# Kernel optimization log

Measured on AMD Instinct MI355X. Metric: run time of the kernel, lower is better.

## Reference

```python
import jax, jax.numpy as jnp
import numpy as np

L, S, N, E, H = 2048, 2048, 4, 512, 8
D = E // H


def _rel_shift(x):
    # Faithful replication of the torch code's _rel_shift (which keeps [:1],
    # collapsing the S axis to size 1): x is (L, N, H, S) -> (L, N, H, 1).
    l, n, h, s = x.shape
    pad = jnp.concatenate([x, jnp.zeros((l, n, h, 1), x.dtype)], axis=-1)  # L,N,H,S+1
    p = jnp.transpose(pad, (0, 3, 1, 2))  # L,S+1,N,H  ('lnhs->lsnh')
    # view([S+1, L, N, H])[:1] == first L*N*H flat elements reshaped to (1,L,N,H)
    p = p.reshape(-1)[: l * n * h].reshape(1, l, n, h)
    return jnp.transpose(p, (1, 2, 3, 0))  # 'slnh->lnhs' -> (L,N,H,1)


def setup_inputs() -> dict:
    key = jax.random.key(0)
    ks = jax.random.split(key, 9)
    sc_in = (2.0 / (E + 3 * E)) ** 0.5  # xavier-ish scale
    sc_sq = (1.0 / E) ** 0.5
    return {
        "query": jax.random.normal(ks[0], (L, N, E), jnp.float32),
        "key": jax.random.normal(ks[1], (S, N, E), jnp.float32),
        "value": jax.random.normal(ks[2], (S, N, E), jnp.float32),
        "sin_pos_enc": jax.random.normal(ks[3], (S, E), jnp.float32),
        "in_proj_weight": jax.random.normal(ks[4], (3 * E, E), jnp.float32) * sc_in,
        "in_proj_bias": jnp.zeros((3 * E,), jnp.float32),
        "out_w": jax.random.normal(ks[5], (E, E), jnp.float32) * sc_sq,
        "out_b": jnp.zeros((E,), jnp.float32),
        "rel_proj_w": jax.random.normal(ks[6], (E, E), jnp.float32) * sc_sq,
        "rel_u": jax.random.normal(ks[7], (H, D), jnp.float32) * 0.1,
        "rel_v": jax.random.normal(ks[8], (H, D), jnp.float32) * 0.1,
    }


def reference(query, key, value, sin_pos_enc, in_proj_weight, in_proj_bias,
              out_w, out_b, rel_proj_w, rel_u, rel_v):
    def src_proj(x, base):
        w = in_proj_weight[base * E:(base + 1) * E]
        b = in_proj_bias[base * E:(base + 1) * E]
        y = x @ w.T + b  # T,N,E
        return y.reshape(y.shape[0], -1, H, D)  # T,N,H,D

    q = src_proj(query, 0)   # L,N,H,D
    k = src_proj(key, 1)     # S,N,H,D
    v = src_proj(value, 2)   # S,N,H,D
    rel_pos = (sin_pos_enc @ rel_proj_w.T).reshape(S, H, D)  # S,H,D

    term_ac = jnp.einsum('lnhd,snhd->lnhs', q + rel_u, k)      # L,N,H,S
    term_bd = jnp.einsum('lnhd,shd->lnhs', q + rel_v, rel_pos) # L,N,H,S
    term_bd = _rel_shift(term_bd)                              # L,N,H,1

    att = jax.nn.softmax((term_ac + term_bd) / (D ** 0.5), axis=-1)  # L,N,H,S
    out = jnp.einsum('lnhs,snhd->lnhd', att, v).reshape(L, -1, E)    # L,N,E
    out = out @ out_w.T + out_b
    att_weights = jnp.transpose(att.mean(axis=-2), (1, 0, 2))  # N,L,S
    return (out, att_weights)
```

## Files before the change

### kernel.cpp

```cpp
#include <hip/hip_runtime.h>
#include <hip/hip_bf16.h>
#include <stdint.h>


#define L_Q 2048
#define S_K 2048
#define N_B 4
#define E_D 512
#define H_N 8
#define D_H 64

typedef unsigned short u16;
typedef unsigned int u32;
typedef short v8s __attribute__((ext_vector_type(8)));
typedef float v4f __attribute__((ext_vector_type(4)));

#define MFMA16(a, b, c) __builtin_amdgcn_mfma_f32_16x16x32_bf16(a, b, c, 0, 0, 0)

__device__ __forceinline__ float bf2f(u16 u) {
  unsigned int x = ((unsigned int)u) << 16;
  return __builtin_bit_cast(float, x);
}
__device__ __forceinline__ u16 f2bf(float f) {
  unsigned int x = __builtin_bit_cast(unsigned int, f);
  x += 0x7FFFu + ((x >> 16) & 1u);
  return (u16)(x >> 16);
}

__device__ __forceinline__ float expfast(float sv) {
  const float x =
      __builtin_amdgcn_fmed3f(sv * 0.18033688011112042f, -43.2809f, 43.2809f);
#if __has_builtin(__builtin_amdgcn_exp2f)
  return __builtin_amdgcn_exp2f(x);
#else
  return __expf(x * 0.6931471805599453f);
#endif
}

__device__ __forceinline__ u32 cvtpk(float lo, float hi) {
  u32 r;
  asm("v_cvt_pk_bf16_f32 %0, %1, %2" : "=v"(r) : "v"(lo), "v"(hi));
  return r;
}

#if __has_builtin(__builtin_amdgcn_global_load_lds)
#define HAVE_GLDS 1
__device__ __forceinline__ void glds16(const u16* g, u16* l) {
  __builtin_amdgcn_global_load_lds(
      (const __attribute__((address_space(1))) void*)g,
      (__attribute__((address_space(3))) void*)l, 16, 0, 0);
}
#else
#define HAVE_GLDS 0
#endif

struct Cvt8 {
  const float* s[8];
  u16* d[8];
};
__global__ __launch_bounds__(256) void cvt_k(Cvt8 a) {
  const size_t t = ((size_t)blockIdx.x * 256 + threadIdx.x) * 4;
  const size_t cum[9] = {0,        4194304,  8388608,  12582912, 13369344,
                         13631488, 13633024, 13633536, 13634048};
  if (t >= cum[8]) return;
  int sg = 0;
#pragma unroll
  for (int i = 1; i < 8; i++) sg += (t >= cum[i]);
  const size_t off = t - cum[sg];
  const v4f x = *(const v4f*)(a.s[sg] + off);
  ushort4 o;
  o.x = f2bf(x[0]);
  o.y = f2bf(x[1]);
  o.z = f2bf(x[2]);
  o.w = f2bf(x[3]);
  *(ushort4*)(a.d[sg] + off) = o;
}

__device__ __forceinline__ void gemm_core(const u16* A, const u16* W, int m0,
                                          int n0, u16* As, u16* Bs,
                                          v4f acc[4][4]) {
  const int lane = threadIdx.x & 63;
  const int w = threadIdx.x >> 6;
  const int wr = w >> 1, wc = w & 1;
  const int q = lane >> 4, c = lane & 15;
#pragma unroll
  for (int i = 0; i < 4; i++)
#pragma unroll
    for (int j = 0; j < 4; j++) acc[i][j] = (v4f){0.f, 0.f, 0.f, 0.f};
  for (int kk = 0; kk < 16; ++kk) {
    const u16* ga = A + (size_t)(m0 + lane) * E_D + kk * 32 + w * 8;
    const u16* gb = W + (size_t)(n0 + lane) * E_D + kk * 32 + w * 8;
#if HAVE_GLDS
    __syncthreads();
    glds16(ga, As + w * 1032);
    glds16(ga + 64 * E_D, As + w * 1032 + 512);
    glds16(gb, Bs + w * 1032);
    glds16(gb + 64 * E_D, Bs + w * 1032 + 512);
    __syncthreads();
#else
    const v8s va0 = *(const v8s*)ga;
    const v8s va1 = *(const v8s*)(ga + 64 * E_D);
    const v8s vb0 = *(const v8s*)gb;
    const v8s vb1 = *(const v8s*)(gb + 64 * E_D);
    __syncthreads();
    *(v8s*)(As + w * 1032 + lane * 8) = va0;
    *(v8s*)(As + w * 1032 + 512 + lane * 8) = va1;
    *(v8s*)(Bs + w * 1032 + lane * 8) = vb0;
    *(v8s*)(Bs + w * 1032 + 512 + lane * 8) = vb1;
    __syncthreads();
#endif
    v8s a[4], b[4];
#pragma unroll
    for (int i = 0; i < 4; i++)
      a[i] = *(const v8s*)(As + q * 1032 + (wr * 64 + i * 16 + c) * 8);
#pragma unroll
    for (int j = 0; j < 4; j++)
      b[j] = *(const v8s*)(Bs + q * 1032 + (wc * 64 + j * 16 + c) * 8);
#pragma unroll
    for (int i = 0; i < 4; i++)
#pragma unroll
      for (int j = 0; j < 4; j++) acc[i][j] = MFMA16(a[i], b[j], acc[i][j]);
  }
}

__global__ __launch_bounds__(256) void gemm_qkv(
    const u16* __restrict__ qb, const u16* __restrict__ kb,
    const u16* __restrict__ vb, const u16* __restrict__ Wallb,
    const u16* __restrict__ biasb, const u16* __restrict__ rel_ub,
    u16* __restrict__ Qw, u16* __restrict__ Kw, u16* __restrict__ Vt) {
  __shared__ __align__(16) u16 As[4 * 1032];
  __shared__ __align__(16) u16 Bs[4 * 1032];
  const int z = blockIdx.z;
  const u16* A = (z == 0) ? qb : ((z == 1) ? kb : vb);
  const int m0 = blockIdx.x * 128, n0 = blockIdx.y * 128;
  v4f acc[4][4];
  gemm_core(A, Wallb + (size_t)z * E_D * E_D, m0, n0, As, Bs, acc);
  const int lane = threadIdx.x & 63, w = threadIdx.x >> 6;
  const int wr = w >> 1, wc = w & 1;
  const int q = lane >> 4, c = lane & 15;
#pragma unroll
  for (int j = 0; j < 4; j++) {
    const int jg = n0 + wc * 64 + j * 16 + c;
    const int h = jg >> 6, d = jg & 63;
    float add =
        bf2f(biasb[z * E_D + jg]) + ((z == 0) ? bf2f(rel_ub[jg]) : 0.f);
#pragma unroll
    for (int i = 0; i < 4; i++) {
#pragma unroll
      for (int r = 0; r < 4; r++) {
        const int mg = m0 + wr * 64 + i * 16 + q * 4 + r;
        const int row = mg >> 2, nn = mg & 3;
        const u16 o = f2bf(acc[i][j][r] + add);
        if (z == 0)
          Qw[((size_t)(nn * H_N + h) * L_Q + row) * D_H + d] = o;
        else if (z == 1)
          Kw[((size_t)(nn * H_N + h) * S_K + row) * D_H + d] = o;
        else
          Vt[((size_t)(nn * H_N + h) * D_H + d) * S_K + row] = o;
      }
    }
  }
}

__global__ __launch_bounds__(256) void gemm_out(const u16* __restrict__ Actx,
                                                const u16* __restrict__ Woutb,
                                                const u16* __restrict__ boutb,
                                                float* __restrict__ out) {
  __shared__ __align__(16) u16 As[4 * 1032];
  __shared__ __align__(16) u16 Bs[4 * 1032];
  const int m0 = blockIdx.x * 128, n0 = blockIdx.y * 128;
  v4f acc[4][4];
  gemm_core(Actx, Woutb, m0, n0, As, Bs, acc);
  const int lane = threadIdx.x & 63, w = threadIdx.x >> 6;
  const int wr = w >> 1, wc = w & 1;
  const int q = lane >> 4, c = lane & 15;
#pragma unroll
  for (int j = 0; j < 4; j++) {
    const int jg = n0 + wc * 64 + j * 16 + c;
    const float bb = bf2f(boutb[jg]);
#pragma unroll
    for (int i = 0; i < 4; i++) {
#pragma unroll
      for (int r = 0; r < 4; r++) {
        const int mg = m0 + wr * 64 + i * 16 + q * 4 + r;
        out[(size_t)mg * E_D + jg] = acc[i][j][r] + bb;
      }
    }
  }
}

__global__ __launch_bounds__(256) void flash_pv(
    const u16* __restrict__ Qw, const u16* __restrict__ Kw,
    const u16* __restrict__ Vt, u16* __restrict__ Actx,
    float* __restrict__ Rbuf) {
  __shared__ __align__(16) u16 Qs[8 * 520];
  __shared__ __align__(16) u16 Ks[8 * 520];
  __shared__ __align__(16) u16 Vs[8 * 520];
  __shared__ __align__(16) u32 PsU[4 * 16 * 36];
  const int lane = threadIdx.x & 63, w = threadIdx.x >> 6;
  const int q = lane >> 4, c = lane & 15;
  const int l0 = blockIdx.x * 64;
  const int nh = blockIdx.z * H_N + blockIdx.y;
  {
    const u16* g = Qw + ((size_t)nh * L_Q + l0 + lane) * D_H + w * 8;
    const v8s vq0 = *(const v8s*)g;
    const v8s vq1 = *(const v8s*)(g + 32);
    *(v8s*)(Qs + w * 520 + lane * 8) = vq0;
    *(v8s*)(Qs + (w + 4) * 520 + lane * 8) = vq1;
  }
  v4f ctx[4];
#pragma unroll
  for (int i = 0; i < 4; i++) ctx[i] = (v4f){0.f, 0.f, 0.f, 0.f};
  float s_run = 0.f;
  __syncthreads();
  const v8s aq0 = *(const v8s*)(Qs + q * 520 + (w * 16 + c) * 8);
  const v8s aq1 = *(const v8s*)(Qs + (q + 4) * 520 + (w * 16 + c) * 8);
  u32* pwU = PsU + w * (16 * 36);
  for (int s0 = 0; s0 < S_K; s0 += 64) {
    const u16* gk = Kw + ((size_t)nh * S_K + s0 + lane) * D_H + w * 8;
    const u16* gv = Vt + ((size_t)nh * D_H + lane) * S_K + s0 + w * 8;
    const v8s vk0 = *(const v8s*)gk;
    const v8s vk1 = *(const v8s*)(gk + 32);
    const v8s vv0 = *(const v8s*)gv;
    const v8s vv1 = *(const v8s*)(gv + 32);
    __syncthreads();
    *(v8s*)(Ks + w * 520 + lane * 8) = vk0;
    *(v8s*)(Ks + (w + 4) * 520 + lane * 8) = vk1;
    *(v8s*)(Vs + w * 520 + lane * 8) = vv0;
    *(v8s*)(Vs + (w + 4) * 520 + lane * 8) = vv1;
    __syncthreads();
#pragma unroll
    for (int jt = 0; jt < 4; jt++) {
      const v8s bk0 = *(const v8s*)(Ks + q * 520 + (jt * 16 + c) * 8);
      const v8s bk1 = *(const v8s*)(Ks + (q + 4) * 520 + (jt * 16 + c) * 8);
      v4f zz = (v4f){0.f, 0.f, 0.f, 0.f};
      zz = MFMA16(bk0, aq0, zz);
      zz = MFMA16(bk1, aq1, zz);
      const float p0 = expfast(zz[0]);
      const float p1 = expfast(zz[1]);
      const float p2 = expfast(zz[2]);
      const float p3 = expfast(zz[3]);
      s_run += (p0 + p1) + (p2 + p3);
      uint2 pk;
      pk.x = cvtpk(p0, p1);
      pk.y = cvtpk(p2, p3);
      *(uint2*)(pwU + c * 36 + jt * 8 + q * 2) = pk;
    }
    __threadfence_block();
    const v8s bp0 = *(const v8s*)(pwU + c * 36 + q * 4);
    const v8s bp1 = *(const v8s*)(pwU + c * 36 + 16 + q * 4);
#pragma unroll
    for (int ds = 0; ds < 4; ds++) {
      const v8s av0 = *(const v8s*)(Vs + q * 520 + (ds * 16 + c) * 8);
      const v8s av1 = *(const v8s*)(Vs + (q + 4) * 520 + (ds * 16 + c) * 8);
      ctx[ds] = MFMA16(av0, bp0, ctx[ds]);
      ctx[ds] = MFMA16(av1, bp1, ctx[ds]);
    }
  }
  float s = s_run;
  s += __shfl_xor(s, 16);
  s += __shfl_xor(s, 32);
  const float rr = 1.0f / s;
  const int l = l0 + w * 16 + c;
#pragma unroll
  for (int ds = 0; ds < 4; ds++) {
    uint2 o;
    o.x = (u32)f2bf(ctx[ds][0] * rr) | ((u32)f2bf(ctx[ds][1] * rr) << 16);
    o.y = (u32)f2bf(ctx[ds][2] * rr) | ((u32)f2bf(ctx[ds][3] * rr) << 16);
    *(uint2*)(Actx + ((size_t)l * N_B + blockIdx.z) * E_D + blockIdx.y * D_H +
              ds * 16 + q * 4) = o;
  }
  if (q == 0) Rbuf[(size_t)nh * L_Q + l] = rr;
}

__global__ __launch_bounds__(256) void attw_k(const u16* __restrict__ Qw,
                                              const u16* __restrict__ Kw,
                                              const float* __restrict__ Rbuf,
                                              float* __restrict__ AW) {
  __shared__ __align__(16) u16 Qs[8 * 520];
  __shared__ __align__(16) u16 Ks[8 * 520];
  const int lane = threadIdx.x & 63, w = threadIdx.x >> 6;
  const int q = lane >> 4, c = lane & 15;
  const int s_base = blockIdx.x * 256;
  const int l0 = blockIdx.y * 64;
  const int n = blockIdx.z;
  v4f aw[4][4];
#pragma unroll
  for (int ss = 0; ss < 4; ss++)
#pragma unroll
    for (int jt = 0; jt < 4; jt++) aw[ss][jt] = (v4f){0.f, 0.f, 0.f, 0.f};
  for (int h = 0; h < H_N; ++h) {
    const int nh = n * H_N + h;
    float rr[4];
#pragma unroll
    for (int r = 0; r < 4; r++)
      rr[r] = Rbuf[(size_t)nh * L_Q + l0 + w * 16 + q * 4 + r];
    v8s aq0, aq1;
    for (int ss = 0; ss < 4; ++ss) {
      const u16* gk =
          Kw + ((size_t)nh * S_K + s_base + ss * 64 + lane) * D_H + w * 8;
      const v8s vk0 = *(const v8s*)gk;
      const v8s vk1 = *(const v8s*)(gk + 32);
      v8s vq0, vq1;
      if (ss == 0) {
        const u16* g = Qw + ((size_t)nh * L_Q + l0 + lane) * D_H + w * 8;
        vq0 = *(const v8s*)g;
        vq1 = *(const v8s*)(g + 32);
      }
      __syncthreads();
      if (ss == 0) {
        *(v8s*)(Qs + w * 520 + lane * 8) = vq0;
        *(v8s*)(Qs + (w + 4) * 520 + lane * 8) = vq1;
      }
      *(v8s*)(Ks + w * 520 + lane * 8) = vk0;
      *(v8s*)(Ks + (w + 4) * 520 + lane * 8) = vk1;
      __syncthreads();
      if (ss == 0) {
        aq0 = *(const v8s*)(Qs + q * 520 + (w * 16 + c) * 8);
        aq1 = *(const v8s*)(Qs + (q + 4) * 520 + (w * 16 + c) * 8);
      }
#pragma unroll
      for (int jt = 0; jt < 4; jt++) {
        const v8s bk0 = *(const v8s*)(Ks + q * 520 + (jt * 16 + c) * 8);
        const v8s bk1 = *(const v8s*)(Ks + (q + 4) * 520 + (jt * 16 + c) * 8);
        v4f zz = (v4f){0.f, 0.f, 0.f, 0.f};
        zz = MFMA16(aq0, bk0, zz);
        zz = MFMA16(aq1, bk1, zz);
#pragma unroll
        for (int r = 0; r < 4; r++)
          aw[ss][jt][r] += expfast(zz[r]) * rr[r];
      }
    }
  }
#pragma unroll
  for (int ss = 0; ss < 4; ss++)
#pragma unroll
    for (int jt = 0; jt < 4; jt++)
#pragma unroll
      for (int r = 0; r < 4; r++) {
        const int l = l0 + w * 16 + q * 4 + r;
        const int s = s_base + ss * 64 + jt * 16 + c;
        AW[((size_t)n * L_Q + l) * S_K + s] = aw[ss][jt][r] * 0.125f;
      }
}

extern "C" void kernel_launch(void* const* d_in, const int* in_sizes, int n_in,
                              void* d_out, int out_size, void* d_ws,
                              size_t ws_size, hipStream_t stream) {
  char* ws = (char*)d_ws;
  u16* Wallb = (u16*)(ws);
  u16* Woutb = (u16*)(ws + 1572864);
  u16* biasb = (u16*)(ws + 2097152);
  u16* boutb = (u16*)(ws + 2100224);
  u16* rel_ub = (u16*)(ws + 2101248);
  u16* Qw = (u16*)(ws + 4194304);
  u16* Kw = (u16*)(ws + 12582912);
  u16* Vt = (u16*)(ws + 20971520);
  float* Rbuf = (float*)(ws + 29360128);

  float* out = (float*)d_out;
  char* sc = (char*)d_out + 16777216;
  u16* qb = (u16*)(sc);
  u16* kb = (u16*)(sc + 8388608);
  u16* vb = (u16*)(sc + 16777216);
  u16* Actx = (u16*)(sc + 25165824);
  float* AW = out + (size_t)L_Q * N_B * E_D;

  Cvt8 a;
  a.s[0] = (const float*)d_in[0];  a.d[0] = qb;
  a.s[1] = (const float*)d_in[1];  a.d[1] = kb;
  a.s[2] = (const float*)d_in[2];  a.d[2] = vb;
  a.s[3] = (const float*)d_in[4];  a.d[3] = Wallb;
  a.s[4] = (const float*)d_in[6];  a.d[4] = Woutb;
  a.s[5] = (const float*)d_in[5];  a.d[5] = biasb;
  a.s[6] = (const float*)d_in[7];  a.d[6] = boutb;
  a.s[7] = (const float*)d_in[9];  a.d[7] = rel_ub;

  hipLaunchKernelGGL(cvt_k, dim3(13315), dim3(256), 0, stream, a);
  hipLaunchKernelGGL(gemm_qkv, dim3(64, 4, 3), dim3(256), 0, stream, qb, kb,
                     vb, Wallb, biasb, rel_ub, Qw, Kw, Vt);
  hipLaunchKernelGGL(flash_pv, dim3(32, 8, 4), dim3(256), 0, stream, Qw, Kw,
                     Vt, Actx, Rbuf);
  hipLaunchKernelGGL(gemm_out, dim3(64, 4, 1), dim3(256), 0, stream, Actx,
                     Woutb, boutb, out);
  hipLaunchKernelGGL(attw_k, dim3(8, 32, 4), dim3(256), 0, stream, Qw, Kw,
                     Rbuf, AW);
}
```

Measured before the change: 314.4 us.

## Rewrite flash_pv with 32x32 MFMA tiles and register-resident P via permlane swap

The attention-context kernel moves from 16x16x32 to 32x32x16 bf16 MFMA. Each block now covers 128 query rows, with 32 per wave, and the Q operand is held in registers instead of LDS. The softmax probabilities are rearranged into the B-operand layout with v_permlane32_swap, so the LDS round trip and fence for P are gone. The grid is flattened to 512 blocks with an XCD-aware index remap, halving the number of blocks that reload K/V. The cost is higher register pressure and fewer blocks to spread across the CUs.

```diff
diff --git a/kernel.cpp b/kernel.cpp
--- a/kernel.cpp
+++ b/kernel.cpp
@@ -14,8 +14,11 @@
 typedef unsigned int u32;
 typedef short v8s __attribute__((ext_vector_type(8)));
 typedef float v4f __attribute__((ext_vector_type(4)));
+typedef float v16f __attribute__((ext_vector_type(16)));
+typedef u32 v4u __attribute__((ext_vector_type(4)));
 
 #define MFMA16(a, b, c) __builtin_amdgcn_mfma_f32_16x16x32_bf16(a, b, c, 0, 0, 0)
+#define MFMA32(a, b, c) __builtin_amdgcn_mfma_f32_32x32x16_bf16(a, b, c, 0, 0, 0)
 
 __device__ __forceinline__ float bf2f(u16 u) {
   unsigned int x = ((unsigned int)u) << 16;
@@ -41,6 +44,10 @@
   u32 r;
   asm("v_cvt_pk_bf16_f32 %0, %1, %2" : "=v"(r) : "v"(lo), "v"(hi));
   return r;
+}
+
+__device__ __forceinline__ void plswap(u32& a, u32& b) {
+  asm volatile("v_permlane32_swap_b32 %0, %1" : "+v"(a), "+v"(b));
 }
 
 #if __has_builtin(__builtin_amdgcn_global_load_lds)
@@ -193,29 +200,25 @@
     const u16* __restrict__ Qw, const u16* __restrict__ Kw,
     const u16* __restrict__ Vt, u16* __restrict__ Actx,
     float* __restrict__ Rbuf) {
-  __shared__ __align__(16) u16 Qs[8 * 520];
   __shared__ __align__(16) u16 Ks[8 * 520];
   __shared__ __align__(16) u16 Vs[8 * 520];
-  __shared__ __align__(16) u32 PsU[4 * 16 * 36];
   const int lane = threadIdx.x & 63, w = threadIdx.x >> 6;
-  const int q = lane >> 4, c = lane & 15;
-  const int l0 = blockIdx.x * 64;
-  const int nh = blockIdx.z * H_N + blockIdx.y;
+  const int ln = lane & 31, hi = lane >> 5;
+  const int orig = (blockIdx.x & 7) * 64 + (blockIdx.x >> 3);
+  const int l0 = (orig & 15) * 128;
+  const int h = (orig >> 4) & 7;
+  const int n = orig >> 7;
+  const int nh = n * H_N + h;
+  v8s aq[4];
   {
-    const u16* g = Qw + ((size_t)nh * L_Q + l0 + lane) * D_H + w * 8;
-    const v8s vq0 = *(const v8s*)g;
-    const v8s vq1 = *(const v8s*)(g + 32);
-    *(v8s*)(Qs + w * 520 + lane * 8) = vq0;
-    *(v8s*)(Qs + (w + 4) * 520 + lane * 8) = vq1;
-  }
-  v4f ctx[4];
-#pragma unroll
-  for (int i = 0; i < 4; i++) ctx[i] = (v4f){0.f, 0.f, 0.f, 0.f};
+    const u16* gq = Qw + ((size_t)nh * L_Q + l0 + w * 32 + ln) * D_H + hi * 8;
+#pragma unroll
+    for (int kt = 0; kt < 4; kt++) aq[kt] = *(const v8s*)(gq + kt * 16);
+  }
+  v16f ctx[2];
+  ctx[0] = (v16f)0.f;
+  ctx[1] = (v16f)0.f;
   float s_run = 0.f;
-  __syncthreads();
-  const v8s aq0 = *(const v8s*)(Qs + q * 520 + (w * 16 + c) * 8);
-  const v8s aq1 = *(const v8s*)(Qs + (q + 4) * 520 + (w * 16 + c) * 8);
-  u32* pwU = PsU + w * (16 * 36);
   for (int s0 = 0; s0 < S_K; s0 += 64) {
     const u16* gk = Kw + ((size_t)nh * S_K + s0 + lane) * D_H + w * 8;
     const u16* gv = Vt + ((size_t)nh * D_H + lane) * S_K + s0 + w * 8;
@@ -229,48 +232,65 @@
     *(v8s*)(Vs + w * 520 + lane * 8) = vv0;
     *(v8s*)(Vs + (w + 4) * 520 + lane * 8) = vv1;
     __syncthreads();
-#pragma unroll
-    for (int jt = 0; jt < 4; jt++) {
-      const v8s bk0 = *(const v8s*)(Ks + q * 520 + (jt * 16 + c) * 8);
-      const v8s bk1 = *(const v8s*)(Ks + (q + 4) * 520 + (jt * 16 + c) * 8);
-      v4f zz = (v4f){0.f, 0.f, 0.f, 0.f};
-      zz = MFMA16(bk0, aq0, zz);
-      zz = MFMA16(bk1, aq1, zz);
-      const float p0 = expfast(zz[0]);
-      const float p1 = expfast(zz[1]);
-      const float p2 = expfast(zz[2]);
-      const float p3 = expfast(zz[3]);
-      s_run += (p0 + p1) + (p2 + p3);
-      uint2 pk;
-      pk.x = cvtpk(p0, p1);
-      pk.y = cvtpk(p2, p3);
-      *(uint2*)(pwU + c * 36 + jt * 8 + q * 2) = pk;
-    }
-    __threadfence_block();
-    const v8s bp0 = *(const v8s*)(pwU + c * 36 + q * 4);
-    const v8s bp1 = *(const v8s*)(pwU + c * 36 + 16 + q * 4);
-#pragma unroll
-    for (int ds = 0; ds < 4; ds++) {
-      const v8s av0 = *(const v8s*)(Vs + q * 520 + (ds * 16 + c) * 8);
-      const v8s av1 = *(const v8s*)(Vs + (q + 4) * 520 + (ds * 16 + c) * 8);
-      ctx[ds] = MFMA16(av0, bp0, ctx[ds]);
-      ctx[ds] = MFMA16(av1, bp1, ctx[ds]);
-    }
-  }
-  float s = s_run;
-  s += __shfl_xor(s, 16);
-  s += __shfl_xor(s, 32);
+    v8s pb[4];
+#pragma unroll
+    for (int st = 0; st < 2; st++) {
+      v16f zz = (v16f)0.f;
+#pragma unroll
+      for (int kt = 0; kt < 4; kt++) {
+        const v8s bk =
+            *(const v8s*)(Ks + (kt * 2 + hi) * 520 + (st * 32 + ln) * 8);
+        zz = MFMA32(bk, aq[kt], zz);
+      }
+      float p[16];
+#pragma unroll
+      for (int r = 0; r < 16; r++) {
+        p[r] = expfast(zz[r]);
+        s_run += p[r];
+      }
+#pragma unroll
+      for (int half = 0; half < 2; half++) {
+        const int rb = half * 8;
+        u32 a0 = cvtpk(p[rb + 0], p[rb + 1]);
+        u32 b0 = cvtpk(p[rb + 4], p[rb + 5]);
+        u32 a1 = cvtpk(p[rb + 2], p[rb + 3]);
+        u32 b1 = cvtpk(p[rb + 6], p[rb + 7]);
+        plswap(a0, b0);
+        plswap(a1, b1);
+        v4u t;
+        t.x = a0;
+        t.y = a1;
+        t.z = b0;
+        t.w = b1;
+        pb[st * 2 + half] = __builtin_bit_cast(v8s, t);
+      }
+    }
+#pragma unroll
+    for (int dt = 0; dt < 2; dt++) {
+#pragma unroll
+      for (int ks = 0; ks < 4; ks++) {
+        const v8s av =
+            *(const v8s*)(Vs + (ks * 2 + hi) * 520 + (dt * 32 + ln) * 8);
+        ctx[dt] = MFMA32(av, pb[ks], ctx[dt]);
+      }
+    }
+  }
+  const float s = s_run + __shfl_xor(s_run, 32);
   const float rr = 1.0f / s;
-  const int l = l0 + w * 16 + c;
-#pragma unroll
-  for (int ds = 0; ds < 4; ds++) {
-    uint2 o;
-    o.x = (u32)f2bf(ctx[ds][0] * rr) | ((u32)f2bf(ctx[ds][1] * rr) << 16);
-    o.y = (u32)f2bf(ctx[ds][2] * rr) | ((u32)f2bf(ctx[ds][3] * rr) << 16);
-    *(uint2*)(Actx + ((size_t)l * N_B + blockIdx.z) * E_D + blockIdx.y * D_H +
-              ds * 16 + q * 4) = o;
-  }
-  if (q == 0) Rbuf[(size_t)nh * L_Q + l] = rr;
+  const int l = l0 + w * 32 + ln;
+  u16* pout = Actx + ((size_t)l * N_B + n) * E_D + h * D_H;
+#pragma unroll
+  for (int dt = 0; dt < 2; dt++) {
+#pragma unroll
+    for (int g = 0; g < 4; g++) {
+      const int d = dt * 32 + g * 8 + hi * 4;
+      uint2 o;
+      o.x = cvtpk(ctx[dt][g * 4 + 0] * rr, ctx[dt][g * 4 + 1] * rr);
+      o.y = cvtpk(ctx[dt][g * 4 + 2] * rr, ctx[dt][g * 4 + 3] * rr);
+      *(uint2*)(pout + d) = o;
+    }
+  }
+  if (hi == 0) Rbuf[(size_t)nh * L_Q + l] = rr;
 }
 
 __global__ __launch_bounds__(256) void attw_k(const u16* __restrict__ Qw,
@@ -379,8 +399,8 @@
   hipLaunchKernelGGL(cvt_k, dim3(13315), dim3(256), 0, stream, a);
   hipLaunchKernelGGL(gemm_qkv, dim3(64, 4, 3), dim3(256), 0, stream, qb, kb,
                      vb, Wallb, biasb, rel_ub, Qw, Kw, Vt);
-  hipLaunchKernelGGL(flash_pv, dim3(32, 8, 4), dim3(256), 0, stream, Qw, Kw,
-                     Vt, Actx, Rbuf);
+  hipLaunchKernelGGL(flash_pv, dim3(512), dim3(256), 0, stream, Qw, Kw, Vt,
+                     Actx, Rbuf);
   hipLaunchKernelGGL(gemm_out, dim3(64, 4, 1), dim3(256), 0, stream, Actx,
                      Woutb, boutb, out);
   hipLaunchKernelGGL(attw_k, dim3(8, 32, 4), dim3(256), 0, stream, Qw, Kw,
```

Measured after the change: 297.5 us. 1.06x faster.
